# Performance work log

Hardware: AMD Instinct MI355X
Metric: run time of the kernel (lower is better)

The kernel has to match this reference:

```python
import jax, jax.numpy as jnp
import numpy as np

N = 30000   # nodes
E = 480000  # edges
C = 64      # in_channels
NC = 101    # num_classes
K1 = 5      # kernel_size per dim
K = K1 * K1 # 25 kernel weight matrices (dim=2)


def _spline_conv(x, src, dst, pseudo, W, root, bias):
    """SplineConv, degree-1 open B-spline, dim=2, kernel_size=5, aggr='mean'.
    x: [N,C_in], pseudo: [E,2] in [0,1], W: [25,C_in,C_out], root: [C_in,C_out].
    """
    n, c = x.shape
    v = pseudo * (K1 - 1)                       # [E,2] in [0, K1-1]
    bot = jnp.clip(jnp.floor(v), 0, K1 - 1)
    frac = v - bot                              # fractional part
    bot_i = bot.astype(jnp.int32)
    bits = jnp.array([[0, 0], [0, 1], [1, 0], [1, 1]], dtype=jnp.int32)  # S=4 combos
    idx_d = jnp.clip(bot_i[:, None, :] + bits[None, :, :], 0, K1 - 1)    # [E,4,2]
    w_d = jnp.where(bits[None, :, :] == 1, frac[:, None, :], 1.0 - frac[:, None, :])
    B = w_d[..., 0] * w_d[..., 1]               # [E,4] basis weights
    kidx = idx_d[..., 0] * K1 + idx_d[..., 1]   # [E,4] flat kernel index in [0,25)
    msg = B[:, :, None] * x[src][:, None, :]    # [E,4,C] weighted source feats
    seg = (dst[:, None] * K + kidx).reshape(-1) # combined (node,kernel) segment id
    acc = jax.ops.segment_sum(msg.reshape(-1, c), seg, num_segments=n * K)
    acc = acc.reshape(n, K, c)                  # [N,25,C]
    out = jnp.einsum('nkc,kcd->nd', acc, W)     # apply kernel weight matrices
    deg = jax.ops.segment_sum(jnp.ones(dst.shape[0], x.dtype), dst, num_segments=n)
    out = out / jnp.maximum(deg, 1.0)[:, None]  # mean aggregation
    out = out + x @ root                        # root weight
    if bias is not None:
        out = out + bias
    return out


def _bn(x, g, b):
    m = x.mean(0)
    v = x.var(0)
    return g * (x - m) * jax.lax.rsqrt(v + 1e-5) + b


def setup_inputs() -> dict:
    key = jax.random.key(0)
    ks = jax.random.split(key, 30)
    p = lambda k, shape: jax.random.normal(k, shape, jnp.float32) * 0.05
    d = {
        'x': jax.random.normal(ks[0], (N, C), jnp.float32),
        'edge_attr': jax.random.uniform(ks[1], (E, 3), dtype=jnp.float32),
        'src': jax.random.randint(ks[2], (E,), 0, N),
        'dst': jax.random.randint(ks[3], (E,), 0, N),
    }
    for i, name in enumerate(['conv1', 'conv2', 'conv3']):
        d[name + '_W'] = p(ks[4 + 2 * i], (K, C, C))
        d[name + '_root'] = p(ks[5 + 2 * i], (C, C))
        d['norm%d_gamma' % (i + 1)] = jnp.ones((C,), jnp.float32)
        d['norm%d_beta' % (i + 1)] = jnp.zeros((C,), jnp.float32)
    for j, (name, oc) in enumerate([('regr', 4), ('cls', NC), ('obj', 1)]):
        d[name + '_W'] = p(ks[10 + 3 * j], (K, C, oc))
        d[name + '_root'] = p(ks[11 + 3 * j], (C, oc))
        d[name + '_bias'] = jnp.zeros((oc,), jnp.float32)
    return d


def reference(x, edge_attr, src, dst,
              conv1_W, conv1_root, norm1_gamma, norm1_beta,
              conv2_W, conv2_root, norm2_gamma, norm2_beta,
              conv3_W, conv3_root, norm3_gamma, norm3_beta,
              regr_W, regr_root, regr_bias,
              cls_W, cls_root, cls_bias,
              obj_W, obj_root, obj_bias):
    pseudo = edge_attr[:, :2]
    x1 = jax.nn.relu(_bn(_spline_conv(x, src, dst, pseudo, conv1_W, conv1_root, None), norm1_gamma, norm1_beta))
    x2 = jax.nn.relu(_bn(_spline_conv(x1, src, dst, pseudo, conv2_W, conv2_root, None), norm2_gamma, norm2_beta))
    x3 = jax.nn.relu(_bn(_spline_conv(x1, src, dst, pseudo, conv3_W, conv3_root, None), norm3_gamma, norm3_beta))
    reg = _spline_conv(x2, src, dst, pseudo, regr_W, regr_root, regr_bias)
    cls = _spline_conv(x3, src, dst, pseudo, cls_W, cls_root, cls_bias)
    obj = _spline_conv(x3, src, dst, pseudo, obj_W, obj_root, obj_bias)
    return (cls, reg, obj)
```

## Files before the change

kernel.cpp:

```cpp
#include <hip/hip_runtime.h>
#include <hip/hip_bf16.h>

#define NN 30000
#define NE 480000
#define CIN 64
#define KD 1600
#define KT 1664
#define KMAC 13
#define BM 64
#define NBLK 469
#define MROWS (NBLK*BM)
#define NBS 118
#define REG_OFF  (30000*101)
#define OBJ_OFF  (30000*105)

typedef short bf16x8 __attribute__((ext_vector_type(8)));
typedef float f32x4  __attribute__((ext_vector_type(4)));
typedef __attribute__((address_space(3))) unsigned lds_u32;
typedef __attribute__((address_space(1))) const unsigned glb_u32;

__device__ __forceinline__ ushort f2bf(float x) {
    union { float f; unsigned u; } v; v.f = x;
    unsigned r = v.u + 0x7FFFu + ((v.u >> 16) & 1u);
    return (ushort)(r >> 16);
}

__global__ void k_count(const int* __restrict__ dst, int* __restrict__ deg) {
    int e = blockIdx.x * 256 + threadIdx.x;
    if (e < NE) atomicAdd(&deg[dst[e]], 1);
}

__global__ void k_scan1(const int* __restrict__ deg, int* __restrict__ bsum) {
    __shared__ int sred[4];
    int i = blockIdx.x * 256 + threadIdx.x;
    int v = (i < NN) ? deg[i] : 0;
    #pragma unroll
    for (int o = 32; o >= 1; o >>= 1) v += __shfl_down(v, o);
    int w = threadIdx.x >> 6, l = threadIdx.x & 63;
    if (l == 0) sred[w] = v;
    __syncthreads();
    if (threadIdx.x == 0) bsum[blockIdx.x] = sred[0] + sred[1] + sred[2] + sred[3];
}

__global__ void k_scan2(const int* __restrict__ bsum, int* __restrict__ boff) {
    __shared__ int s[128];
    int t = threadIdx.x;
    int v = (t < NBS) ? bsum[t] : 0;
    s[t] = v; __syncthreads();
    for (int o = 1; o < 128; o <<= 1) {
        int u = (t >= o) ? s[t - o] : 0;
        __syncthreads(); s[t] += u; __syncthreads();
    }
    if (t < NBS) boff[t] = s[t] - v;
}

__global__ void k_scan3(const int* __restrict__ deg, const int* __restrict__ boff,
                        int* __restrict__ rp, int* __restrict__ cur, float* __restrict__ invd) {
    __shared__ int s[256];
    int t = threadIdx.x;
    int i = blockIdx.x * 256 + t;
    int v = (i < NN) ? deg[i] : 0;
    s[t] = v; __syncthreads();
    for (int o = 1; o < 256; o <<= 1) {
        int u = (t >= o) ? s[t - o] : 0;
        __syncthreads(); s[t] += u; __syncthreads();
    }
    int ex = s[t] - v + boff[blockIdx.x];
    if (i < NN) {
        rp[i] = ex; cur[i] = ex;
        invd[i] = 1.f / (float)(v > 0 ? v : 1);
    }
    if (i == NN - 1) rp[NN] = NE;
}

__global__ void k_scatter(const float* __restrict__ ea, const int* __restrict__ src,
                          const int* __restrict__ dst, int* __restrict__ cur,
                          float4* __restrict__ mB, int2* __restrict__ mI) {
    int e = blockIdx.x * 256 + threadIdx.x;
    if (e >= NE) return;
    float p0 = ea[e*3+0], p1 = ea[e*3+1];
    float v0 = p0*4.f, v1 = p1*4.f;
    float b0 = fminf(fmaxf(floorf(v0),0.f),4.f);
    float b1 = fminf(fmaxf(floorf(v1),0.f),4.f);
    float f0 = v0-b0, f1 = v1-b1;
    int i0 = (int)b0, i1 = (int)b1;
    float B00 = (1.f-f0)*(1.f-f1);
    float B01 = (1.f-f0)*f1;
    float B10 = f0*(1.f-f1);
    float B11 = f0*f1;
    int k00 = i0*5 + i1;
    int dn = dst[e];
    int pos = atomicAdd(&cur[dn], 1);
    mB[pos] = make_float4(B00,B01,B10,B11);
    mI[pos] = make_int2(k00, src[e]);
}

__global__ void k_prepw(const float* W1,const float* R1,const float* W2,const float* R2,
                        const float* W3,const float* R3,const float* Wr,const float* Rr,
                        const float* Wc,const float* Rc,const float* Wo,const float* Ro,
                        ushort* T1, ushort* T23, ushort* Tr, ushort* TcTo) {
    int b = blockIdx.x;
    const float* W; const float* R; ushort* T; int od; int col;
    if      (b < 64)  { W=W1; R=R1; T=T1  + (long)b*KT;       od=64;  col=b;     }
    else if (b < 128) { W=W2; R=R2; T=T23 + (long)(b-64)*KT;  od=64;  col=b-64;  }
    else if (b < 192) { W=W3; R=R3; T=T23 + (long)(b-64)*KT;  od=64;  col=b-128; }
    else if (b < 208) { W=Wr; R=Rr; T=Tr  + (long)(b-192)*KT; od=4;   col=b-192; }
    else if (b < 320) { W=Wc; R=Rc; T=TcTo+ (long)(b-208)*KT; od=101; col=b-208; }
    else              { W=Wo; R=Ro; T=TcTo+ (long)(b-208)*KT; od=1;   col=b-320; }
    for (int kc = threadIdx.x; kc < KT; kc += 256) {
        float v = 0.f;
        if (col < od) v = (kc < KD) ? W[(long)kc*od + col] : R[(long)(kc-KD)*od + col];
        T[kc] = f2bf(v);
    }
}

#define AGGC(K, A_, B_, C_, D_) case K: A_ += bb.x*xu; B_ += bb.y*xu; C_ += bb.z*xu; D_ += bb.w*xu; break;

template<bool NORM>
__global__ void k_agg(const int* __restrict__ rp, const float4* __restrict__ mB,
                      const int2* __restrict__ mI, const float* __restrict__ f,
                      const float* __restrict__ invd,
                      const float* __restrict__ st, const float* __restrict__ g,
                      const float* __restrict__ be, ushort* __restrict__ A) {
    int wid = (blockIdx.x * 256 + threadIdx.x) >> 6;
    wid = __builtin_amdgcn_readfirstlane(wid);
    int l = threadIdx.x & 63;
    if (wid >= NN) return;
    float na = 0.f, nc = 0.f;
    if (NORM) {
        const float inv_n = 1.f / (float)NN;
        float mm = st[l] * inv_n;
        float var = st[64 + l] * inv_n - mm * mm;
        float rs = rsqrtf(var + 1e-5f);
        na = g[l] * rs; nc = be[l] - mm * na;
    }
    float a00=0.f,a01=0.f,a02=0.f,a03=0.f,a04=0.f;
    float a05=0.f,a06=0.f,a07=0.f,a08=0.f,a09=0.f;
    float a10=0.f,a11=0.f,a12=0.f,a13=0.f,a14=0.f;
    float a15=0.f,a16=0.f,a17=0.f,a18=0.f,a19=0.f;
    float a20=0.f,a21=0.f,a22=0.f,a23=0.f,a24=0.f;
    int beg = rp[wid], end = rp[wid + 1];
    for (int e0 = beg; e0 < end; e0 += 8) {
        int2 m[8];
        #pragma unroll
        for (int u = 0; u < 8; ++u) {
            int e = e0 + u;
            m[u] = mI[(e < end) ? e : beg];
        }
        float xv[8];
        #pragma unroll
        for (int u = 0; u < 8; ++u) xv[u] = f[(long)m[u].y * CIN + l];
        __builtin_amdgcn_sched_barrier(0);
        float4 b[8];
        #pragma unroll
        for (int u = 0; u < 8; ++u) {
            int e = e0 + u;
            b[u] = mB[(e < end) ? e : beg];
            if (e >= end) b[u] = make_float4(0,0,0,0);
        }
        __builtin_amdgcn_sched_barrier(0);
        #pragma unroll
        for (int u = 0; u < 8; ++u) {
            float xu = xv[u];
            if (NORM) xu = fmaxf(xu * na + nc, 0.f);
            int k00 = __builtin_amdgcn_readfirstlane(m[u].x);
            float4 bb = b[u];
            switch (k00) {
                AGGC(0,  a00,a01,a05,a06)
                AGGC(1,  a01,a02,a06,a07)
                AGGC(2,  a02,a03,a07,a08)
                AGGC(3,  a03,a04,a08,a09)
                AGGC(5,  a05,a06,a10,a11)
                AGGC(6,  a06,a07,a11,a12)
                AGGC(7,  a07,a08,a12,a13)
                AGGC(8,  a08,a09,a13,a14)
                AGGC(10, a10,a11,a15,a16)
                AGGC(11, a11,a12,a16,a17)
                AGGC(12, a12,a13,a17,a18)
                AGGC(13, a13,a14,a18,a19)
                AGGC(15, a15,a16,a20,a21)
                AGGC(16, a16,a17,a21,a22)
                AGGC(17, a17,a18,a22,a23)
                AGGC(18, a18,a19,a23,a24)
                default: break;
            }
        }
    }
    float s = invd[wid];
    ushort* rb = A + (long)wid * KT + l;
    #define STO(K, V) rb[K*CIN] = f2bf((V) * s);
    STO(0,a00)  STO(1,a01)  STO(2,a02)  STO(3,a03)  STO(4,a04)
    STO(5,a05)  STO(6,a06)  STO(7,a07)  STO(8,a08)  STO(9,a09)
    STO(10,a10) STO(11,a11) STO(12,a12) STO(13,a13) STO(14,a14)
    STO(15,a15) STO(16,a16) STO(17,a17) STO(18,a18) STO(19,a19)
    STO(20,a20) STO(21,a21) STO(22,a22) STO(23,a23) STO(24,a24)
    #undef STO
    float rv = f[(long)wid * CIN + l];
    if (NORM) rv = fmaxf(rv * na + nc, 0.f);
    rb[KD] = f2bf(rv);
}

template<int MODE>
__global__ void k_gemm(const ushort* __restrict__ A, const ushort* __restrict__ B,
                       float* __restrict__ o0, float* __restrict__ o1,
                       float* __restrict__ s0, float* __restrict__ s1,
                       const float* __restrict__ b0, const float* __restrict__ b1) {
    __shared__ ushort As[2 * 8192];
    f32x4* part = (f32x4*)As;
    const int tid = threadIdx.x, w = tid >> 6, l = tid & 63;
    const int m0 = blockIdx.x * BM;

    int colrow;
    if constexpr (MODE == 0)      colrow = ((w & 3) << 4) + (l & 15);
    else if constexpr (MODE == 2) colrow = (l & 15);
    else                          colrow = (w << 4) + (l & 15);
    const ushort* Bp = B + (long)colrow * KT + ((l >> 4) << 3);

    const int row0 = (w << 3) + (l >> 4);
    const int row1 = row0 + 4;
    const ushort* g0 = A + (long)(m0 + row0) * KT + (((l & 15) ^ (row0 & 7)) << 3);
    const ushort* g1 = A + (long)(m0 + row1) * KT + (((l & 15) ^ (row1 & 7)) << 3);
    ushort* d0 = (ushort*)As + (w << 10);
    ushort* d1 = d0 + 512;

    auto stage = [&](int ks, int bf) {
        const ushort* sA = g0 + ks * 128;
        const ushort* sB = g1 + ks * 128;
        ushort* dA = d0 + (bf << 13);
        ushort* dB = d1 + (bf << 13);
        __builtin_amdgcn_global_load_lds((glb_u32*)sA, (lds_u32*)dA, 16, 0, 0);
        __builtin_amdgcn_global_load_lds((glb_u32*)sB, (lds_u32*)dB, 16, 0, 0);
    };

    f32x4 acc[4];
    #pragma unroll
    for (int m = 0; m < 4; ++m) acc[m] = (f32x4){0.f,0.f,0.f,0.f};

    stage(0, 0);
    __syncthreads();

    int buf = 0;
    for (int ks = 0; ks < KMAC; ++ks) {
        if (ks < KMAC - 1) stage(ks + 1, buf ^ 1);
        bool act;
        if constexpr (MODE == 0)      act = (w < 4) ? (ks < 7) : (ks >= 7);
        else if constexpr (MODE == 2) act = ((ks & 7) == w);
        else                          act = true;
        if (act) {
            const char* Ab = (const char*)As + buf * 16384;
            #pragma unroll
            for (int s = 0; s < 4; ++s) {
                bf16x8 bb = *(const bf16x8*)(Bp + ks * 128 + s * 32);
                #pragma unroll
                for (int m = 0; m < 4; ++m) {
                    int r = (m << 4) + (l & 15);
                    int j = (s << 2) + (l >> 4);
                    bf16x8 a = *(const bf16x8*)(Ab + r * 256 + ((j ^ (r & 7)) << 4));
                    acc[m] = __builtin_amdgcn_mfma_f32_16x16x32_bf16(a, bb, acc[m], 0, 0, 0);
                }
            }
        }
        __syncthreads();
        buf ^= 1;
    }

    auto emit = [&](f32x4* ac, float* out, int ostride, int col, int odcap, float bv, float* stats) {
        float p1 = 0.f, p2 = 0.f;
        #pragma unroll
        for (int m = 0; m < 4; ++m) {
            #pragma unroll
            for (int r = 0; r < 4; ++r) {
                int row = m0 + (m << 4) + ((l >> 4) << 2) + r;
                if (row < NN) {
                    float v = ac[m][r] + bv;
                    if (col < odcap) out[(long)row * ostride + col] = v;
                    p1 += v; p2 += v * v;
                }
            }
        }
        if (stats) {
            p1 += __shfl_down(p1, 32); p2 += __shfl_down(p2, 32);
            p1 += __shfl_down(p1, 16); p2 += __shfl_down(p2, 16);
            if (l < 16) { atomicAdd(&stats[col], p1); atomicAdd(&stats[64 + col], p2); }
        }
    };

    if constexpr (MODE == 0) {
        if (w >= 4) {
            #pragma unroll
            for (int m = 0; m < 4; ++m) part[((w & 3) << 8) + (l << 2) + m] = acc[m];
        }
        __syncthreads();
        if (w < 4) {
            #pragma unroll
            for (int m = 0; m < 4; ++m) acc[m] += part[((w & 3) << 8) + (l << 2) + m];
            emit(acc, o0, 64, ((w & 3) << 4) + (l & 15), 64, 0.f, s0);
        }
    } else if constexpr (MODE == 1) {
        if (w < 4) emit(acc, o0, 64, (w << 4) + (l & 15), 64, 0.f, s0);
        else       emit(acc, o1, 64, ((w - 4) << 4) + (l & 15), 64, 0.f, s1);
    } else if constexpr (MODE == 2) {
        if (w > 0) {
            #pragma unroll
            for (int m = 0; m < 4; ++m) part[((w - 1) << 8) + (l << 2) + m] = acc[m];
        }
        __syncthreads();
        if (w == 0) {
            for (int i = 0; i < 7; ++i) {
                #pragma unroll
                for (int m = 0; m < 4; ++m) acc[m] += part[(i << 8) + (l << 2) + m];
            }
            int col = l & 15;
            emit(acc, o0, 4, col, 4, (col < 4) ? b0[col] : 0.f, nullptr);
        }
    } else {
        if (w < 7) {
            int col = (w << 4) + (l & 15);
            emit(acc, o0, 101, col, 101, (col < 101) ? b0[col] : 0.f, nullptr);
        } else {
            int col = l & 15;
            emit(acc, o1, 1, col, 1, b1[0], nullptr);
        }
    }
}

extern "C" void kernel_launch(void* const* d_in, const int* in_sizes, int n_in,
                              void* d_out, int out_size, void* d_ws, size_t ws_size,
                              hipStream_t stream) {
    const float* x    = (const float*)d_in[0];
    const float* ea   = (const float*)d_in[1];
    const int*   src  = (const int*)d_in[2];
    const int*   dst  = (const int*)d_in[3];
    const float* W1   = (const float*)d_in[4];
    const float* R1   = (const float*)d_in[5];
    const float* g1   = (const float*)d_in[6];
    const float* be1  = (const float*)d_in[7];
    const float* W2   = (const float*)d_in[8];
    const float* R2   = (const float*)d_in[9];
    const float* g2   = (const float*)d_in[10];
    const float* be2  = (const float*)d_in[11];
    const float* W3   = (const float*)d_in[12];
    const float* R3   = (const float*)d_in[13];
    const float* g3   = (const float*)d_in[14];
    const float* be3  = (const float*)d_in[15];
    const float* Wr   = (const float*)d_in[16];
    const float* Rr   = (const float*)d_in[17];
    const float* br   = (const float*)d_in[18];
    const float* Wc   = (const float*)d_in[19];
    const float* Rc   = (const float*)d_in[20];
    const float* bc   = (const float*)d_in[21];
    const float* Wo   = (const float*)d_in[22];
    const float* Ro   = (const float*)d_in[23];
    const float* bo   = (const float*)d_in[24];
    float* out = (float*)d_out;

    char* p = (char*)d_ws;
    auto alloc = [&](size_t bytes) { char* r = p; p += (bytes + 255) & ~(size_t)255; return r; };
    float4* mB   = (float4*)alloc((size_t)NE * 16);
    int2*   mI   = (int2*)  alloc((size_t)NE * 8);
    int*    deg  = (int*)   alloc((size_t)NN * 4);
    int*    rp   = (int*)   alloc((size_t)(NN + 1) * 4);
    int*    cur  = (int*)   alloc((size_t)NN * 4);
    float*  invd = (float*) alloc((size_t)NN * 4);
    int*    bsum = (int*)   alloc((size_t)NBS * 4);
    int*    boff = (int*)   alloc((size_t)NBS * 4);
    ushort* T1   = (ushort*)alloc((size_t)64  * KT * 2);
    ushort* T23  = (ushort*)alloc((size_t)128 * KT * 2);
    ushort* Tr   = (ushort*)alloc((size_t)16  * KT * 2);
    ushort* TcTo = (ushort*)alloc((size_t)128 * KT * 2);
    float*  y1   = (float*) alloc((size_t)NN * CIN * 4);
    float*  y2   = (float*) alloc((size_t)NN * CIN * 4);
    float*  y3   = (float*) alloc((size_t)NN * CIN * 4);
    float*  stats= (float*) alloc(3 * 128 * 4);
    ushort* A    = (ushort*)alloc((size_t)MROWS * KT * 2);
    float* st1 = stats, *st2 = stats + 128, *st3 = stats + 256;

    hipMemsetAsync(deg, 0, (size_t)NN * 4, stream);
    hipMemsetAsync(stats, 0, 3 * 128 * 4, stream);

    k_count  <<<1875, 256, 0, stream>>>(dst, deg);
    k_scan1  <<<NBS, 256, 0, stream>>>(deg, bsum);
    k_scan2  <<<1, 128, 0, stream>>>(bsum, boff);
    k_scan3  <<<NBS, 256, 0, stream>>>(deg, boff, rp, cur, invd);
    k_scatter<<<1875, 256, 0, stream>>>(ea, src, dst, cur, mB, mI);
    k_prepw  <<<336, 256, 0, stream>>>(W1,R1,W2,R2,W3,R3,Wr,Rr,Wc,Rc,Wo,Ro,T1,T23,Tr,TcTo);

    k_agg<false><<<7500, 256, 0, stream>>>(rp, mB, mI, x, invd, nullptr, nullptr, nullptr, A);
    k_gemm<0><<<NBLK, 512, 0, stream>>>(A, T1, y1, nullptr, st1, nullptr, nullptr, nullptr);
    k_agg<true><<<7500, 256, 0, stream>>>(rp, mB, mI, y1, invd, st1, g1, be1, A);
    k_gemm<1><<<NBLK, 512, 0, stream>>>(A, T23, y2, y3, st2, st3, nullptr, nullptr);
    k_agg<true><<<7500, 256, 0, stream>>>(rp, mB, mI, y2, invd, st2, g2, be2, A);
    k_gemm<2><<<NBLK, 512, 0, stream>>>(A, Tr, out + REG_OFF, nullptr, nullptr, nullptr, br, nullptr);
    k_agg<true><<<7500, 256, 0, stream>>>(rp, mB, mI, y3, invd, st3, g3, be3, A);
    k_gemm<3><<<NBLK, 512, 0, stream>>>(A, TcTo, out, out + OBJ_OFF, nullptr, nullptr, bc, bo);
}
```

Measured before the change: 392.4 us.

## Pre-normalize features to bf16 before gather-aggregation, shrinking gather traffic

Result: slower. 468.8 us (+19.5%).

```diff
diff --git a/kernel.cpp b/kernel.cpp
--- a/kernel.cpp
+++ b/kernel.cpp
@@ -23,6 +23,9 @@
     union { float f; unsigned u; } v; v.f = x;
     unsigned r = v.u + 0x7FFFu + ((v.u >> 16) & 1u);
     return (ushort)(r >> 16);
+}
+__device__ __forceinline__ float bf2f(ushort u) {
+    union { unsigned i; float f; } v; v.i = ((unsigned)u) << 16; return v.f;
 }
 
 __global__ void k_count(const int* __restrict__ dst, int* __restrict__ deg) {
@@ -114,26 +117,35 @@
     }
 }
 
+__global__ void k_cvt(const float* __restrict__ x, ushort* __restrict__ xb) {
+    int idx = blockIdx.x * 1024 + threadIdx.x;
+    if (idx < NN*CIN) xb[idx] = f2bf(x[idx]);
+}
+
+__global__ void k_norm(const float* __restrict__ y, const float* __restrict__ st,
+                       const float* __restrict__ g, const float* __restrict__ be,
+                       ushort* __restrict__ xb) {
+    int idx = blockIdx.x * 1024 + threadIdx.x;
+    if (idx >= NN*CIN) return;
+    int d = idx & 63;
+    const float inv_n = 1.f / (float)NN;
+    float m = st[d] * inv_n;
+    float var = st[64 + d] * inv_n - m * m;
+    float a = g[d] * rsqrtf(var + 1e-5f);
+    float c = be[d] - m * a;
+    xb[idx] = f2bf(fmaxf(y[idx] * a + c, 0.f));
+}
+
 #define AGGC(K, A_, B_, C_, D_) case K: A_ += bb.x*xu; B_ += bb.y*xu; C_ += bb.z*xu; D_ += bb.w*xu; break;
 
-template<bool NORM>
-__global__ void k_agg(const int* __restrict__ rp, const float4* __restrict__ mB,
-                      const int2* __restrict__ mI, const float* __restrict__ f,
-                      const float* __restrict__ invd,
-                      const float* __restrict__ st, const float* __restrict__ g,
-                      const float* __restrict__ be, ushort* __restrict__ A) {
-    int wid = (blockIdx.x * 256 + threadIdx.x) >> 6;
+__global__ __launch_bounds__(1024) void k_agg(
+                      const int* __restrict__ rp, const float4* __restrict__ mB,
+                      const int2* __restrict__ mI, const ushort* __restrict__ f,
+                      const float* __restrict__ invd, ushort* __restrict__ A) {
+    int wid = (blockIdx.x * 1024 + threadIdx.x) >> 6;
     wid = __builtin_amdgcn_readfirstlane(wid);
     int l = threadIdx.x & 63;
     if (wid >= NN) return;
-    float na = 0.f, nc = 0.f;
-    if (NORM) {
-        const float inv_n = 1.f / (float)NN;
-        float mm = st[l] * inv_n;
-        float var = st[64 + l] * inv_n - mm * mm;
-        float rs = rsqrtf(var + 1e-5f);
-        na = g[l] * rs; nc = be[l] - mm * na;
-    }
     float a00=0.f,a01=0.f,a02=0.f,a03=0.f,a04=0.f;
     float a05=0.f,a06=0.f,a07=0.f,a08=0.f,a09=0.f;
     float a10=0.f,a11=0.f,a12=0.f,a13=0.f,a14=0.f;
@@ -147,7 +159,7 @@
             int e = e0 + u;
             m[u] = mI[(e < end) ? e : beg];
         }
-        float xv[8];
+        ushort xv[8];
         #pragma unroll
         for (int u = 0; u < 8; ++u) xv[u] = f[(long)m[u].y * CIN + l];
         __builtin_amdgcn_sched_barrier(0);
@@ -161,8 +173,7 @@
         __builtin_amdgcn_sched_barrier(0);
         #pragma unroll
         for (int u = 0; u < 8; ++u) {
-            float xu = xv[u];
-            if (NORM) xu = fmaxf(xu * na + nc, 0.f);
+            float xu = bf2f(xv[u]);
             int k00 = __builtin_amdgcn_readfirstlane(m[u].x);
             float4 bb = b[u];
             switch (k00) {
@@ -195,9 +206,7 @@
     STO(15,a15) STO(16,a16) STO(17,a17) STO(18,a18) STO(19,a19)
     STO(20,a20) STO(21,a21) STO(22,a22) STO(23,a23) STO(24,a24)
     #undef STO
-    float rv = f[(long)wid * CIN + l];
-    if (NORM) rv = fmaxf(rv * na + nc, 0.f);
-    rb[KD] = f2bf(rv);
+    rb[KD] = f[(long)wid * CIN + l];
 }
 
 template<int MODE>
@@ -371,6 +380,7 @@
     float*  y1   = (float*) alloc((size_t)NN * CIN * 4);
     float*  y2   = (float*) alloc((size_t)NN * CIN * 4);
     float*  y3   = (float*) alloc((size_t)NN * CIN * 4);
+    ushort* xb   = (ushort*)alloc((size_t)NN * CIN * 2);
     float*  stats= (float*) alloc(3 * 128 * 4);
     ushort* A    = (ushort*)alloc((size_t)MROWS * KT * 2);
     float* st1 = stats, *st2 = stats + 128, *st3 = stats + 256;
@@ -384,13 +394,17 @@
     k_scan3  <<<NBS, 256, 0, stream>>>(deg, boff, rp, cur, invd);
     k_scatter<<<1875, 256, 0, stream>>>(ea, src, dst, cur, mB, mI);
     k_prepw  <<<336, 256, 0, stream>>>(W1,R1,W2,R2,W3,R3,Wr,Rr,Wc,Rc,Wo,Ro,T1,T23,Tr,TcTo);
-
-    k_agg<false><<<7500, 256, 0, stream>>>(rp, mB, mI, x, invd, nullptr, nullptr, nullptr, A);
+    k_cvt    <<<1875, 1024, 0, stream>>>(x, xb);
+
+    k_agg    <<<1875, 1024, 0, stream>>>(rp, mB, mI, xb, invd, A);
     k_gemm<0><<<NBLK, 512, 0, stream>>>(A, T1, y1, nullptr, st1, nullptr, nullptr, nullptr);
-    k_agg<true><<<7500, 256, 0, stream>>>(rp, mB, mI, y1, invd, st1, g1, be1, A);
+    k_norm   <<<1875, 1024, 0, stream>>>(y1, st1, g1, be1, xb);
+    k_agg    <<<1875, 1024, 0, stream>>>(rp, mB, mI, xb, invd, A);
     k_gemm<1><<<NBLK, 512, 0, stream>>>(A, T23, y2, y3, st2, st3, nullptr, nullptr);
-    k_agg<true><<<7500, 256, 0, stream>>>(rp, mB, mI, y2, invd, st2, g2, be2, A);
+    k_norm   <<<1875, 1024, 0, stream>>>(y2, st2, g2, be2, xb);
+    k_agg    <<<1875, 1024, 0, stream>>>(rp, mB, mI, xb, invd, A);
     k_gemm<2><<<NBLK, 512, 0, stream>>>(A, Tr, out + REG_OFF, nullptr, nullptr, nullptr, br, nullptr);
-    k_agg<true><<<7500, 256, 0, stream>>>(rp, mB, mI, y3, invd, st3, g3, be3, A);
+    k_norm   <<<1875, 1024, 0, stream>>>(y3, st3, g3, be3, xb);
+    k_agg    <<<1875, 1024, 0, stream>>>(rp, mB, mI, xb, invd, A);
     k_gemm<3><<<NBLK, 512, 0, stream>>>(A, TcTo, out, out + OBJ_OFF, nullptr, nullptr, bc, bo);
 }
```
